# Optimization experiments

Hardware: AMD Instinct MI355X
Metric: run time of the kernel (lower is better)

Reference implementation:

```python
import math
import jax, jax.numpy as jnp
import numpy as np

L, B, N, D, H, DFF = 4, 64, 511, 256, 8, 512
S = N + 1          # +1 game token
HD = D // H
BW = 7             # BOARD_WIDTH (undefined global in source; board-game policy width)


def layer_norm(x, g, b):
    m = jnp.mean(x, axis=-1, keepdims=True)
    v = jnp.var(x, axis=-1, keepdims=True)
    return (x - m) / jnp.sqrt(v + 1e-5) * g + b


def setup_inputs() -> dict:
    key = jax.random.key(0)
    ks = jax.random.split(key, 24)

    def p(k, shape):
        return jax.random.normal(k, shape, jnp.float32) * 0.02

    return {
        "cell_states": jax.random.randint(ks[0], (B * N,), 0, 3, dtype=jnp.int32),
        "edge_type_matrix": jax.random.randint(ks[1], (B, N, N), 0, 3, dtype=jnp.int32),
        "patch_emb": p(ks[2], (3, D)),
        "game_token": p(ks[3], (1, 1, D)),
        "edge_emb": p(ks[4], (3, H)),   # zeros in source init; random here to exercise bias path
        "in_w": p(ks[5], (L, 3 * D, D)), "in_b": p(ks[6], (L, 3 * D)),
        "out_w": p(ks[7], (L, D, D)), "out_b": p(ks[8], (L, D)),
        "ff1_w": p(ks[9], (L, DFF, D)), "ff1_b": p(ks[10], (L, DFF)),
        "ff2_w": p(ks[11], (L, D, DFF)), "ff2_b": p(ks[12], (L, D)),
        "ln1_g": jnp.ones((L, D)), "ln1_b": jnp.zeros((L, D)),
        "ln2_g": jnp.ones((L, D)), "ln2_b": jnp.zeros((L, D)),
        "fc1_w": p(ks[13], (64, D)), "fc1_b": p(ks[14], (64,)),
        "pol_w": p(ks[15], (BW, 64)), "pol_b": p(ks[16], (BW,)),
        "val_w": p(ks[17], (1, 64)), "val_b": p(ks[18], (1,)),
    }


def reference(cell_states, edge_type_matrix, patch_emb, game_token, edge_emb,
              in_w, in_b, out_w, out_b, ff1_w, ff1_b, ff2_w, ff2_b,
              ln1_g, ln1_b, ln2_g, ln2_b, fc1_w, fc1_b, pol_w, pol_b, val_w, val_b):
    # embed cells and prepend game token -> [B, S, D]
    x = patch_emb[cell_states].reshape(B, N, D)
    x = jnp.concatenate([jnp.broadcast_to(game_token, (B, 1, D)), x], axis=1)

    # edge bias: [B,N,N,H] -> [B,H,N,N], pad token row/col with zeros -> [B,H,S,S]
    bias = jnp.transpose(edge_emb[edge_type_matrix], (0, 3, 1, 2))
    bias = jnp.pad(bias, ((0, 0), (0, 0), (1, 0), (1, 0)))

    scale = math.sqrt(HD)
    for i in range(L):
        h = layer_norm(x, ln1_g[i], ln1_b[i])
        qkv = h @ in_w[i].T + in_b[i]                       # [B,S,3D]
        q, k, v = jnp.split(qkv, 3, axis=-1)
        q = q.reshape(B, S, H, HD).transpose(0, 2, 1, 3)    # [B,H,S,HD]
        k = k.reshape(B, S, H, HD).transpose(0, 2, 1, 3)
        v = v.reshape(B, S, H, HD).transpose(0, 2, 1, 3)
        scores = jnp.einsum('bhqd,bhkd->bhqk', q, k) / scale + bias
        attn = jax.nn.softmax(scores, axis=-1)              # dropout = identity (eval)
        o = jnp.einsum('bhqk,bhkd->bhqd', attn, v)
        o = o.transpose(0, 2, 1, 3).reshape(B, S, D)
        x = x + (o @ out_w[i].T + out_b[i])
        h2 = layer_norm(x, ln2_g[i], ln2_b[i])
        x = x + (jax.nn.relu(h2 @ ff1_w[i].T + ff1_b[i]) @ ff2_w[i].T + ff2_b[i])

    g = x[:, 0, :]
    o = jax.nn.relu(g @ fc1_w.T + fc1_b)
    policy_logits = o @ pol_w.T + pol_b
    value = jnp.tanh(o @ val_w.T + val_b)
    return policy_logits, value
```

## Files before the change

### kernel.cpp

```cpp
#include <hip/hip_runtime.h>
#include <hip/hip_bf16.h>
#include <math.h>

#define L_ 4
#define B_ 64
#define N_ 511
#define D_ 256
#define H_ 8
#define DFF_ 512
#define S_ 512
#define HD_ 32
#define BW_ 7
#define BS_ (B_*S_)

typedef __attribute__((ext_vector_type(8))) short short8;
typedef __attribute__((ext_vector_type(4))) short short4v;
typedef __attribute__((ext_vector_type(4))) float f32x4;

#define L2E 1.44269504088896340f
#define QSCL (0.17677669529663687f * 1.44269504088896340f)

#if defined(__HIP_DEVICE_COMPILE__)
#if __has_builtin(__builtin_amdgcn_mfma_f32_16x16x16bf16_1k)
#define MFMA16(p, v, c) __builtin_amdgcn_mfma_f32_16x16x16bf16_1k(p, v, c, 0, 0, 0)
#elif __has_builtin(__builtin_amdgcn_mfma_f32_16x16x16_bf16)
#define MFMA16(p, v, c) __builtin_amdgcn_mfma_f32_16x16x16_bf16(p, v, c, 0, 0, 0)
#else
#define MFMA16(p, v, c) (c)
#endif
#else
#define MFMA16(p, v, c) (c)
#endif

#if defined(__HIP_DEVICE_COMPILE__) && __has_builtin(__builtin_amdgcn_exp2f)
#define EXP2(x) __builtin_amdgcn_exp2f(x)
#else
#define EXP2(x) exp2f(x)
#endif

__device__ inline ushort f2b(float f) {
    unsigned u = __float_as_uint(f);
    unsigned r = (u + 0x7fffu + ((u >> 16) & 1u)) >> 16;
    return (ushort)r;
}

#if defined(__HIP_DEVICE_COMPILE__) && __has_builtin(__builtin_amdgcn_cvt_pk_bf16_f32)
typedef __attribute__((ext_vector_type(2))) __bf16 bf16x2_t;
__device__ inline uint pk_bf16(float a, float b) {
    bf16x2_t r = __builtin_amdgcn_cvt_pk_bf16_f32(a, b);
    return *(uint*)&r;
}
#else
__device__ inline uint pk_bf16(float a, float b) {
    return (uint)f2b(a) | ((uint)f2b(b) << 16);
}
#endif

__device__ inline f32x4 bsel4v(uint E, uint tlo, uint thi) {
    f32x4 r;
#if defined(__HIP_DEVICE_COMPILE__) && __has_builtin(__builtin_amdgcn_perm)
    uint E2  = E + E;
    uint E2b = E2 | 0x01010101u;
    uint s01 = __builtin_amdgcn_perm(E2b, E2, 0x05010400u);
    uint s23 = __builtin_amdgcn_perm(E2b, E2, 0x07030602u);
    uint p01 = __builtin_amdgcn_perm(thi, tlo, s01);
    uint p23 = __builtin_amdgcn_perm(thi, tlo, s23);
    r[0] = __uint_as_float(p01 << 16);
    r[1] = __uint_as_float(p01 & 0xFFFF0000u);
    r[2] = __uint_as_float(p23 << 16);
    r[3] = __uint_as_float(p23 & 0xFFFF0000u);
#else
    #pragma unroll
    for (int i = 0; i < 4; i++) {
        unsigned char e = (unsigned char)((E >> (8 * i)) & 0xff);
        uint bb = e == 0 ? (tlo & 0xFFFFu) : (e == 1 ? (tlo >> 16) :
                  (e == 2 ? (thi & 0xFFFFu) : 0u));
        r[i] = __uint_as_float(bb << 16);
    }
#endif
    return r;
}

__device__ inline void gload16(const void* g, void* l) {
#if __has_builtin(__builtin_amdgcn_global_load_lds)
    __builtin_amdgcn_global_load_lds(
        (const __attribute__((address_space(1))) void*)g,
        (__attribute__((address_space(3))) void*)l, 16, 0, 0);
#else
    *(short8*)l = *(const short8*)g;
#endif
}

__global__ __launch_bounds__(256) void build_x(const int* __restrict__ cs,
                                               const float* __restrict__ patch,
                                               const float* __restrict__ game,
                                               float* __restrict__ x)
{
    int idx = blockIdx.x * 256 + threadIdx.x;
    int row = idx / (D_ / 4);
    int c4  = idx % (D_ / 4);
    int s = row & (S_ - 1);
    float4 v;
    if (s == 0) {
        v = ((const float4*)game)[c4];
    } else {
        int b = row / S_;
        int cell = cs[b * N_ + s - 1];
        v = ((const float4*)(patch + cell * D_))[c4];
    }
    ((float4*)x)[idx] = v;
}

__global__ __launch_bounds__(256) void build_et8(const int* __restrict__ et,
                                                 unsigned char* __restrict__ et8)
{
    long idx = (long)blockIdx.x * 256 + threadIdx.x;
    int k = (int)(idx & (S_ - 1));
    long rem = idx >> 9;
    int q = (int)(rem & (S_ - 1));
    int b = (int)(rem >> 9);
    unsigned char v = 3;
    if (q > 0 && k > 0) {
        v = (unsigned char)et[((long)b * N_ + (q - 1)) * N_ + (k - 1)];
    }
    et8[idx] = v;
}

__global__ __launch_bounds__(256) void convert_f2b(const float* __restrict__ in,
                                                   ushort* __restrict__ out, int n4)
{
    int i = blockIdx.x * 256 + threadIdx.x;
    if (i >= n4) return;
    float4 v = ((const float4*)in)[i];
    ushort4 o4;
    o4.x = f2b(v.x); o4.y = f2b(v.y); o4.z = f2b(v.z); o4.w = f2b(v.w);
    ((ushort4*)out)[i] = o4;
}

__global__ __launch_bounds__(256) void convert_inw(const float* __restrict__ in,
                                                   ushort* __restrict__ out)
{
    int i = blockIdx.x * 256 + threadIdx.x;
    if (i >= 196608) return;
    float4 v = ((const float4*)in)[i];
    int r = (i >> 6) % 768;
    float s = (r < 256) ? (float)QSCL : 1.f;
    ushort4 o4;
    o4.x = f2b(v.x * s); o4.y = f2b(v.y * s); o4.z = f2b(v.z * s); o4.w = f2b(v.w * s);
    ((ushort4*)out)[i] = o4;
}

__global__ __launch_bounds__(256) void ln_kernel(const float* __restrict__ in,
                                                 ushort* __restrict__ out,
                                                 const float* __restrict__ gw,
                                                 const float* __restrict__ bw)
{
    int t = threadIdx.x;
    int lane = t & 63;
    int r = t >> 6;
    size_t row = (size_t)blockIdx.x * 4 + r;
    float4 v = *(const float4*)(in + row * D_ + lane * 4);
    float s = v.x + v.y + v.z + v.w;
    #pragma unroll
    for (int o = 32; o >= 1; o >>= 1) s += __shfl_xor(s, o);
    float mean = s * (1.f / 256.f);
    float dx = v.x - mean, dy = v.y - mean, dz = v.z - mean, dw = v.w - mean;
    float s2 = dx * dx + dy * dy + dz * dz + dw * dw;
    #pragma unroll
    for (int o = 32; o >= 1; o >>= 1) s2 += __shfl_xor(s2, o);
    float rstd = rsqrtf(s2 * (1.f / 256.f) + 1e-5f);
    float4 g  = *(const float4*)(gw + lane * 4);
    float4 bb = *(const float4*)(bw + lane * 4);
    ushort4 o4;
    o4.x = f2b(dx * rstd * g.x + bb.x);
    o4.y = f2b(dy * rstd * g.y + bb.y);
    o4.z = f2b(dz * rstd * g.z + bb.z);
    o4.w = f2b(dw * rstd * g.w + bb.w);
    *(ushort4*)(out + row * D_ + lane * 4) = o4;
}

template<int K, int NT, bool RELU, bool QSC, bool QKV>
__global__ __launch_bounds__(256, 2) void gemm_lds(const ushort* __restrict__ A,
                                                   const ushort* __restrict__ W,
                                                   const float* __restrict__ bias,
                                                   ushort* __restrict__ Cout,
                                                   ushort* __restrict__ Kb,
                                                   ushort* __restrict__ Vt)
{
    __shared__ ushort As[4096];
    __shared__ ushort Ws[4096];
    const int N = NT * 128;
    int t = threadIdx.x;
    int wave = t >> 6, lane = t & 63;
    int lr = lane & 15, quad = lane >> 4;
    int lk = quad * 8;
    int blk = blockIdx.x;
    int xcd = blk & 7, idx = blk >> 3;
    int m0 = (xcd * 32 + (idx & 31)) * 128;
    int n0 = (idx >> 5) * 128;
    int mh = (wave >> 1) * 64, nh = (wave & 1) * 64;

    const ushort* ga0 = A + (size_t)(m0 + (t >> 2)) * K + (t & 3) * 8;
    const ushort* ga1 = ga0 + (size_t)64 * K;
    const ushort* gw0 = W + (size_t)(n0 + (t >> 2)) * K + (t & 3) * 8;
    const ushort* gw1 = gw0 + (size_t)64 * K;
    ushort* la0 = As + t * 8;
    ushort* la1 = As + t * 8 + 2048;
    ushort* lw0 = Ws + t * 8;
    ushort* lw1 = Ws + t * 8 + 2048;

    f32x4 acc[4][4];
    f32x4 zz = {0.f, 0.f, 0.f, 0.f};
    #pragma unroll
    for (int i = 0; i < 4; i++)
        #pragma unroll
        for (int j = 0; j < 4; j++) acc[i][j] = zz;

    for (int k0 = 0; k0 < K; k0 += 32) {
        gload16(ga0 + k0, la0);
        gload16(ga1 + k0, la1);
        gload16(gw0 + k0, lw0);
        gload16(gw1 + k0, lw1);
        __syncthreads();
        short8 af[4], wf[4];
        #pragma unroll
        for (int i = 0; i < 4; i++) af[i] = *(const short8*)&As[(mh + i * 16 + lr) * 32 + lk];
        #pragma unroll
        for (int j = 0; j < 4; j++) wf[j] = *(const short8*)&Ws[(nh + j * 16 + lr) * 32 + lk];
        #pragma unroll
        for (int i = 0; i < 4; i++)
            #pragma unroll
            for (int j = 0; j < 4; j++)
                acc[i][j] = __builtin_amdgcn_mfma_f32_16x16x32_bf16(af[i], wf[j], acc[i][j], 0, 0, 0);
        __syncthreads();
    }

    #pragma unroll
    for (int nt = 0; nt < 4; nt++) {
        int colbase = n0 + nh + nt * 16;
        int col = colbase + lr;
        float bv = bias[col];
        if (QSC && colbase < 256) bv *= (float)QSCL;
        int region = QKV ? (colbase >> 8) : 0;
        #pragma unroll
        for (int mt = 0; mt < 4; mt++) {
            int rowb = m0 + mh + mt * 16 + quad * 4;
            if (!QKV || region == 0) {
                #pragma unroll
                for (int r = 0; r < 4; r++) {
                    size_t cidx = (size_t)(rowb + r) * N + col;
                    float v = acc[mt][nt][r] + bv;
                    if (RELU) v = fmaxf(v, 0.f);
                    Cout[cidx] = f2b(v);
                }
            } else if (region == 1) {
                int hh = (col >> 5) & 7, d = col & 31;
                int bb = rowb >> 9, s = rowb & 511;
                size_t kbase = ((size_t)(bb * 8 + hh) * 512 + s) * 32 + d;
                #pragma unroll
                for (int r = 0; r < 4; r++)
                    Kb[kbase + (size_t)r * 32] = f2b(acc[mt][nt][r] + bv);
            } else {
                int hh = (col >> 5) & 7, d = col & 31;
                int bb = rowb >> 9, s = rowb & 511;
                ushort4 w;
                w.x = f2b(acc[mt][nt][0] + bv);
                w.y = f2b(acc[mt][nt][1] + bv);
                w.z = f2b(acc[mt][nt][2] + bv);
                w.w = f2b(acc[mt][nt][3] + bv);
                size_t vidx = (((size_t)(bb * 8 + hh) * 32 + (s >> 4)) * 32 + d) * 16 + (s & 15);
                *(ushort4*)&Vt[vidx] = w;
            }
        }
    }
}

template<int K>
__global__ __launch_bounds__(256, 2) void gemm_ln(const ushort* __restrict__ A,
                                                  const ushort* __restrict__ W,
                                                  const float* __restrict__ bias,
                                                  float* __restrict__ X,
                                                  const float* __restrict__ lng,
                                                  const float* __restrict__ lnb,
                                                  ushort* __restrict__ Hout)
{
    __shared__ ushort As[64 * 32];
    __shared__ ushort Ws[256 * 32];
    __shared__ float lds_s[64][4];
    __shared__ float lds_q[64][4];
    int t = threadIdx.x;
    int wave = t >> 6, lane = t & 63;
    int lr = lane & 15, quad = lane >> 4;
    int lk = quad * 8;
    int blk = blockIdx.x;
    int xcd = blk & 7;
    int m0 = (xcd * 64 + (blk >> 3)) * 64;
    int nh = wave * 64;

    const ushort* ga = A + (size_t)(m0 + (t >> 2)) * K + (t & 3) * 8;
    const ushort* gw = W + (size_t)(t >> 2) * K + (t & 3) * 8;
    ushort* la = As + t * 8;
    ushort* lw = Ws + t * 8;

    f32x4 acc[4][4];
    f32x4 zz = {0.f, 0.f, 0.f, 0.f};
    #pragma unroll
    for (int i = 0; i < 4; i++)
        #pragma unroll
        for (int j = 0; j < 4; j++) acc[i][j] = zz;

    for (int k0 = 0; k0 < K; k0 += 32) {
        gload16(ga + k0, la);
        #pragma unroll
        for (int j = 0; j < 4; j++)
            gload16(gw + (size_t)(j * 64) * K + k0, lw + j * 2048);
        __syncthreads();
        short8 af[4], wf[4];
        #pragma unroll
        for (int i = 0; i < 4; i++) af[i] = *(const short8*)&As[(i * 16 + lr) * 32 + lk];
        #pragma unroll
        for (int j = 0; j < 4; j++) wf[j] = *(const short8*)&Ws[(nh + j * 16 + lr) * 32 + lk];
        #pragma unroll
        for (int i = 0; i < 4; i++)
            #pragma unroll
            for (int j = 0; j < 4; j++)
                acc[i][j] = __builtin_amdgcn_mfma_f32_16x16x32_bf16(af[i], wf[j], acc[i][j], 0, 0, 0);
        __syncthreads();
    }

    float gc[4], bc[4], bi[4];
    #pragma unroll
    for (int nt = 0; nt < 4; nt++) {
        int col = nh + nt * 16 + lr;
        gc[nt] = lng[col]; bc[nt] = lnb[col]; bi[nt] = bias[col];
    }
    float psum[16], psq[16];
    #pragma unroll
    for (int e = 0; e < 16; e++) { psum[e] = 0.f; psq[e] = 0.f; }
    #pragma unroll
    for (int nt = 0; nt < 4; nt++) {
        #pragma unroll
        for (int mt = 0; mt < 4; mt++) {
            #pragma unroll
            for (int r = 0; r < 4; r++) {
                int row = m0 + mt * 16 + quad * 4 + r;
                size_t idx = (size_t)row * D_ + nh + nt * 16 + lr;
                float v = acc[mt][nt][r] + bi[nt] + X[idx];
                X[idx] = v;
                acc[mt][nt][r] = v;
                psum[mt * 4 + r] += v;
                psq[mt * 4 + r]  += v * v;
            }
        }
    }
    #pragma unroll
    for (int e = 0; e < 16; e++) {
        float s = psum[e], q = psq[e];
        s += __shfl_xor(s, 1); q += __shfl_xor(q, 1);
        s += __shfl_xor(s, 2); q += __shfl_xor(q, 2);
        s += __shfl_xor(s, 4); q += __shfl_xor(q, 4);
        s += __shfl_xor(s, 8); q += __shfl_xor(q, 8);
        psum[e] = s; psq[e] = q;
    }
    if (lr == 0) {
        #pragma unroll
        for (int mt = 0; mt < 4; mt++)
            #pragma unroll
            for (int r = 0; r < 4; r++) {
                int rl = mt * 16 + quad * 4 + r;
                lds_s[rl][wave] = psum[mt * 4 + r];
                lds_q[rl][wave] = psq[mt * 4 + r];
            }
    }
    __syncthreads();
    #pragma unroll
    for (int mt = 0; mt < 4; mt++) {
        #pragma unroll
        for (int r = 0; r < 4; r++) {
            int rl = mt * 16 + quad * 4 + r;
            f32x4 ss = *(const f32x4*)lds_s[rl];
            f32x4 qq = *(const f32x4*)lds_q[rl];
            float s = ss[0] + ss[1] + ss[2] + ss[3];
            float q = qq[0] + qq[1] + qq[2] + qq[3];
            float mean = s * (1.f / 256.f);
            float rstd = rsqrtf(q * (1.f / 256.f) - mean * mean + 1e-5f);
            int row = m0 + mt * 16 + quad * 4 + r;
            #pragma unroll
            for (int nt = 0; nt < 4; nt++) {
                size_t idx = (size_t)row * D_ + nh + nt * 16 + lr;
                float hv = (acc[mt][nt][r] - mean) * rstd * gc[nt] + bc[nt];
                Hout[idx] = f2b(hv);
            }
        }
    }
}

__global__ __launch_bounds__(256, 8) void attn_mfma(const ushort* __restrict__ qkv,
                                                    const ushort* __restrict__ Kb,
                                                    const ushort* __restrict__ Vt,
                                                    const unsigned char* __restrict__ et8,
                                                    const float* __restrict__ eemb,
                                                    ushort* __restrict__ o)
{
    __shared__ unsigned char Est[2][2][2048];
    int t = threadIdx.x;
    int wave = t >> 6, lane = t & 63;
    int lr = lane & 15, quad = lane >> 4;
    int lk = quad * 8;
    int blk = blockIdx.x;
    int b = ((blk >> 8) << 3) | (blk & 7);
    int h = (blk >> 3) & 7;
    int qq = (blk >> 6) & 3;
    int bh = b * 8 + h;
    int q0 = qq * 128 + wave * 32;
    float eb0 = eemb[h] * L2E, eb1 = eemb[8 + h] * L2E, eb2 = eemb[16 + h] * L2E;
    uint tlo = (uint)f2b(eb0) | ((uint)f2b(eb1) << 16);
    uint thi = (uint)f2b(eb2);

    short8 qf[2];
    #pragma unroll
    for (int X = 0; X < 2; X++)
        qf[X] = *(const short8*)(qkv + ((size_t)(b * S_ + q0 + X * 16 + lr)) * 768 + h * 32 + lk);
    const ushort* Kp = Kb + ((size_t)(bh * S_ + lr)) * 32 + lk;
    const ushort* Vp = Vt + (size_t)bh * 32 * 512 + lr * 16 + quad * 4;
    int ehalf = wave >> 1;
    int erow = ((wave & 1) << 6) | lane;
    const unsigned char* Ep = et8 + ((size_t)(b * S_ + qq * 128 + erow)) * S_ + ehalf * 16;
    unsigned char* ElD = &Est[0][ehalf][erow * 16];

    const short4v vones = { (short)0x3F80, (short)0x3F80, (short)0x3F80, (short)0x3F80 };

    f32x4 zz = {0.f, 0.f, 0.f, 0.f};
    f32x4 oacc[2][2], lacc[2];
    #pragma unroll
    for (int X = 0; X < 2; X++) { oacc[X][0] = zz; oacc[X][1] = zz; lacc[X] = zz; }

    gload16(Ep, ElD);
    short8 kf0 = *(const short8*)(Kp);
    short8 kf1 = *(const short8*)(Kp + 16 * 32);
    __syncthreads();

    for (int k0 = 0; k0 < S_; k0 += 32) {
        int cb = (k0 >> 5) & 1, nb = cb ^ 1;
        if (k0 < S_ - 32) {
            gload16(Ep + k0 + 32, ElD + (size_t)nb * 4096);
        }
        int kn = (k0 + 32) & (S_ - 1);
        short8 nk0 = *(const short8*)(Kp + (size_t)kn * 32);
        short8 nk1 = *(const short8*)(Kp + (size_t)(kn + 16) * 32);
        const ushort* vt0 = Vp + (size_t)(k0 >> 4) * 512;
        short4v vf00 = *(const short4v*)(vt0);
        short4v vf01 = *(const short4v*)(vt0 + 256);
        short4v vf10 = *(const short4v*)(vt0 + 512);
        short4v vf11 = *(const short4v*)(vt0 + 768);
        #pragma unroll
        for (int X = 0; X < 2; X++) {
            int qrow = wave * 32 + X * 16 + lr;
            uint E0 = *(const uint*)&Est[cb][0][qrow * 16 + quad * 4];
            uint E1 = *(const uint*)&Est[cb][1][qrow * 16 + quad * 4];
            f32x4 c0 = bsel4v(E0, tlo, thi);
            f32x4 c1 = bsel4v(E1, tlo, thi);
            f32x4 s0 = __builtin_amdgcn_mfma_f32_16x16x32_bf16(kf0, qf[X], c0, 0, 0, 0);
            f32x4 s1 = __builtin_amdgcn_mfma_f32_16x16x32_bf16(kf1, qf[X], c1, 0, 0, 0);
            float p0[4], p1[4];
            #pragma unroll
            for (int r = 0; r < 4; r++) {
                p0[r] = EXP2(s0[r]);
                p1[r] = EXP2(s1[r]);
            }
            union { short4v v; uint2 u; } P0, P1;
            P0.u.x = pk_bf16(p0[0], p0[1]); P0.u.y = pk_bf16(p0[2], p0[3]);
            P1.u.x = pk_bf16(p1[0], p1[1]); P1.u.y = pk_bf16(p1[2], p1[3]);
            oacc[X][0] = MFMA16(P0.v, vf00, oacc[X][0]);
            oacc[X][1] = MFMA16(P0.v, vf01, oacc[X][1]);
            lacc[X]    = MFMA16(P0.v, vones, lacc[X]);
            oacc[X][0] = MFMA16(P1.v, vf10, oacc[X][0]);
            oacc[X][1] = MFMA16(P1.v, vf11, oacc[X][1]);
            lacc[X]    = MFMA16(P1.v, vones, lacc[X]);
        }
        kf0 = nk0; kf1 = nk1;
        __syncthreads();
    }

    #pragma unroll
    for (int X = 0; X < 2; X++) {
        #pragma unroll
        for (int r = 0; r < 4; r++) {
            int q = quad * 4 + r;
            float inv = 1.f / lacc[X][r];
            size_t base = (size_t)(b * S_ + q0 + X * 16 + q) * D_ + h * 32;
            o[base + lr]      = f2b(oacc[X][0][r] * inv);
            o[base + 16 + lr] = f2b(oacc[X][1][r] * inv);
        }
    }
}

__global__ __launch_bounds__(64) void head_kernel(const float* __restrict__ x,
                                                  const float* __restrict__ fc1w,
                                                  const float* __restrict__ fc1b,
                                                  const float* __restrict__ polw,
                                                  const float* __restrict__ polb,
                                                  const float* __restrict__ valw,
                                                  const float* __restrict__ valb,
                                                  float* __restrict__ out)
{
    __shared__ float o1[64];
    int b = blockIdx.x;
    int t = threadIdx.x;
    const float* g = x + (size_t)b * S_ * D_;
    float acc = fc1b[t];
    for (int k = 0; k < D_; k++) acc += g[k] * fc1w[t * D_ + k];
    o1[t] = fmaxf(acc, 0.f);
    __syncthreads();
    if (t < BW_) {
        float a = polb[t];
        for (int k = 0; k < 64; k++) a += o1[k] * polw[t * 64 + k];
        out[b * BW_ + t] = a;
    } else if (t == BW_) {
        float a = valb[0];
        for (int k = 0; k < 64; k++) a += o1[k] * valw[k];
        out[B_ * BW_ + b] = tanhf(a);
    }
}

extern "C" void kernel_launch(void* const* d_in, const int* in_sizes, int n_in,
                              void* d_out, int out_size, void* d_ws, size_t ws_size,
                              hipStream_t stream)
{
    const int*   cs    = (const int*)d_in[0];
    const int*   etm   = (const int*)d_in[1];
    const float* patch = (const float*)d_in[2];
    const float* game  = (const float*)d_in[3];
    const float* eemb  = (const float*)d_in[4];
    const float* in_w  = (const float*)d_in[5];
    const float* in_b  = (const float*)d_in[6];
    const float* out_w = (const float*)d_in[7];
    const float* out_b = (const float*)d_in[8];
    const float* ff1_w = (const float*)d_in[9];
    const float* ff1_b = (const float*)d_in[10];
    const float* ff2_w = (const float*)d_in[11];
    const float* ff2_b = (const float*)d_in[12];
    const float* ln1_g = (const float*)d_in[13];
    const float* ln1_b = (const float*)d_in[14];
    const float* ln2_g = (const float*)d_in[15];
    const float* ln2_b = (const float*)d_in[16];
    const float* fc1_w = (const float*)d_in[17];
    const float* fc1_b = (const float*)d_in[18];
    const float* pol_w = (const float*)d_in[19];
    const float* pol_b = (const float*)d_in[20];
    const float* val_w = (const float*)d_in[21];
    const float* val_b = (const float*)d_in[22];
    float* out = (float*)d_out;

    char* base = (char*)d_ws;
    float*  x     = (float*)(base + 0);
    ushort* h     = (ushort*)(base + 33554432);
    ushort* qkvb  = (ushort*)(base + 50331648);
    ushort* Kb    = (ushort*)(base + 100663296);
    ushort* Vt    = (ushort*)(base + 117440512);
    ushort* ob    = (ushort*)(base + 134217728);
    unsigned char* et8 = (unsigned char*)(base + 150994944);
    ushort* inwb  = (ushort*)(base + 167772160);
    ushort* outwb = (ushort*)(base + 169345024);
    ushort* ff1wb = (ushort*)(base + 169869312);
    ushort* ff2wb = (ushort*)(base + 170917888);

    build_x<<<8192, 256, 0, stream>>>(cs, patch, game, x);
    build_et8<<<65536, 256, 0, stream>>>(etm, et8);
    convert_inw<<<768, 256, 0, stream>>>(in_w, inwb);
    convert_f2b<<<256, 256, 0, stream>>>(out_w, outwb, 65536);
    convert_f2b<<<512, 256, 0, stream>>>(ff1_w, ff1wb, 131072);
    convert_f2b<<<512, 256, 0, stream>>>(ff2_w, ff2wb, 131072);

    ln_kernel<<<8192, 256, 0, stream>>>(x, h, ln1_g, ln1_b);

    for (int i = 0; i < L_; i++) {
        gemm_lds<256, 6, false, true, true><<<1536, 256, 0, stream>>>(
            h, inwb + (size_t)i * 196608, in_b + i * 768, qkvb, Kb, Vt);
        attn_mfma<<<2048, 256, 0, stream>>>(qkvb, Kb, Vt, et8, eemb, ob);
        gemm_ln<256><<<512, 256, 0, stream>>>(
            ob, outwb + (size_t)i * 65536, out_b + i * 256, x,
            ln2_g + i * D_, ln2_b + i * D_, h);
        gemm_lds<256, 4, true, false, false><<<1024, 256, 0, stream>>>(
            h, ff1wb + (size_t)i * 131072, ff1_b + i * 512, qkvb, nullptr, nullptr);
        int nx = (i + 1 < L_) ? (i + 1) : i;
        gemm_ln<512><<<512, 256, 0, stream>>>(
            qkvb, ff2wb + (size_t)i * 131072, ff2_b + i * 256, x,
            ln1_g + nx * D_, ln1_b + nx * D_, h);
    }
    head_kernel<<<B_, 64, 0, stream>>>(x, fc1_w, fc1_b, pol_w, pol_b, val_w, val_b, out);
}
```

Baseline: 801.7 us.

## Use 16x16x32 MFMA for PV with permuted K rows and direct edge loads

Result: slower. 1.993 ms (+148.6%).

```diff
diff --git a/kernel.cpp b/kernel.cpp
--- a/kernel.cpp
+++ b/kernel.cpp
@@ -19,18 +19,6 @@
 
 #define L2E 1.44269504088896340f
 #define QSCL (0.17677669529663687f * 1.44269504088896340f)
-
-#if defined(__HIP_DEVICE_COMPILE__)
-#if __has_builtin(__builtin_amdgcn_mfma_f32_16x16x16bf16_1k)
-#define MFMA16(p, v, c) __builtin_amdgcn_mfma_f32_16x16x16bf16_1k(p, v, c, 0, 0, 0)
-#elif __has_builtin(__builtin_amdgcn_mfma_f32_16x16x16_bf16)
-#define MFMA16(p, v, c) __builtin_amdgcn_mfma_f32_16x16x16_bf16(p, v, c, 0, 0, 0)
-#else
-#define MFMA16(p, v, c) (c)
-#endif
-#else
-#define MFMA16(p, v, c) (c)
-#endif
 
 #if defined(__HIP_DEVICE_COMPILE__) && __has_builtin(__builtin_amdgcn_exp2f)
 #define EXP2(x) __builtin_amdgcn_exp2f(x)
@@ -402,7 +390,6 @@
                                                     const float* __restrict__ eemb,
                                                     ushort* __restrict__ o)
 {
-    __shared__ unsigned char Est[2][2][2048];
     int t = threadIdx.x;
     int wave = t >> 6, lane = t & 63;
     int lr = lane & 15, quad = lane >> 4;
@@ -421,45 +408,40 @@
     #pragma unroll
     for (int X = 0; X < 2; X++)
         qf[X] = *(const short8*)(qkv + ((size_t)(b * S_ + q0 + X * 16 + lr)) * 768 + h * 32 + lk);
-    const ushort* Kp = Kb + ((size_t)(bh * S_ + lr)) * 32 + lk;
-    const ushort* Vp = Vt + (size_t)bh * 32 * 512 + lr * 16 + quad * 4;
-    int ehalf = wave >> 1;
-    int erow = ((wave & 1) << 6) | lane;
-    const unsigned char* Ep = et8 + ((size_t)(b * S_ + qq * 128 + erow)) * S_ + ehalf * 16;
-    unsigned char* ElD = &Est[0][ehalf][erow * 16];
-
-    const short4v vones = { (short)0x3F80, (short)0x3F80, (short)0x3F80, (short)0x3F80 };
+    int gl = ((lr >> 2) << 3) | (lr & 3);
+    const ushort* Kp = Kb + ((size_t)(bh * S_) + gl) * 32 + lk;
+    const ushort* Vp = Vt + (size_t)bh * 16384 + (quad >> 1) * 512 + lr * 16 + (quad & 1) * 8;
+    const unsigned char* Ep0 = et8 + ((size_t)(b * S_ + q0 + lr)) * 512 + quad * 8;
+    const unsigned char* Ep1 = Ep0 + (size_t)16 * 512;
+
+    const short8 vones8 = { (short)0x3F80, (short)0x3F80, (short)0x3F80, (short)0x3F80,
+                            (short)0x3F80, (short)0x3F80, (short)0x3F80, (short)0x3F80 };
 
     f32x4 zz = {0.f, 0.f, 0.f, 0.f};
     f32x4 oacc[2][2], lacc[2];
     #pragma unroll
     for (int X = 0; X < 2; X++) { oacc[X][0] = zz; oacc[X][1] = zz; lacc[X] = zz; }
 
-    gload16(Ep, ElD);
     short8 kf0 = *(const short8*)(Kp);
-    short8 kf1 = *(const short8*)(Kp + 16 * 32);
-    __syncthreads();
+    short8 kf1 = *(const short8*)(Kp + 128);
+    uint2 e0 = *(const uint2*)(Ep0);
+    uint2 e1 = *(const uint2*)(Ep1);
 
     for (int k0 = 0; k0 < S_; k0 += 32) {
-        int cb = (k0 >> 5) & 1, nb = cb ^ 1;
-        if (k0 < S_ - 32) {
-            gload16(Ep + k0 + 32, ElD + (size_t)nb * 4096);
-        }
         int kn = (k0 + 32) & (S_ - 1);
         short8 nk0 = *(const short8*)(Kp + (size_t)kn * 32);
-        short8 nk1 = *(const short8*)(Kp + (size_t)(kn + 16) * 32);
+        short8 nk1 = *(const short8*)(Kp + (size_t)kn * 32 + 128);
+        uint2 ne0 = *(const uint2*)(Ep0 + kn);
+        uint2 ne1 = *(const uint2*)(Ep1 + kn);
         const ushort* vt0 = Vp + (size_t)(k0 >> 4) * 512;
-        short4v vf00 = *(const short4v*)(vt0);
-        short4v vf01 = *(const short4v*)(vt0 + 256);
-        short4v vf10 = *(const short4v*)(vt0 + 512);
-        short4v vf11 = *(const short4v*)(vt0 + 768);
+        short8 vb0 = *(const short8*)(vt0);
+        short8 vb1 = *(const short8*)(vt0 + 256);
         #pragma unroll
         for (int X = 0; X < 2; X++) {
-            int qrow = wave * 32 + X * 16 + lr;
-            uint E0 = *(const uint*)&Est[cb][0][qrow * 16 + quad * 4];
-            uint E1 = *(const uint*)&Est[cb][1][qrow * 16 + quad * 4];
-            f32x4 c0 = bsel4v(E0, tlo, thi);
-            f32x4 c1 = bsel4v(E1, tlo, thi);
+            uint Ea = X ? e1.x : e0.x;
+            uint Eb = X ? e1.y : e0.y;
+            f32x4 c0 = bsel4v(Ea, tlo, thi);
+            f32x4 c1 = bsel4v(Eb, tlo, thi);
             f32x4 s0 = __builtin_amdgcn_mfma_f32_16x16x32_bf16(kf0, qf[X], c0, 0, 0, 0);
             f32x4 s1 = __builtin_amdgcn_mfma_f32_16x16x32_bf16(kf1, qf[X], c1, 0, 0, 0);
             float p0[4], p1[4];
@@ -468,18 +450,14 @@
                 p0[r] = EXP2(s0[r]);
                 p1[r] = EXP2(s1[r]);
             }
-            union { short4v v; uint2 u; } P0, P1;
-            P0.u.x = pk_bf16(p0[0], p0[1]); P0.u.y = pk_bf16(p0[2], p0[3]);
-            P1.u.x = pk_bf16(p1[0], p1[1]); P1.u.y = pk_bf16(p1[2], p1[3]);
-            oacc[X][0] = MFMA16(P0.v, vf00, oacc[X][0]);
-            oacc[X][1] = MFMA16(P0.v, vf01, oacc[X][1]);
-            lacc[X]    = MFMA16(P0.v, vones, lacc[X]);
-            oacc[X][0] = MFMA16(P1.v, vf10, oacc[X][0]);
-            oacc[X][1] = MFMA16(P1.v, vf11, oacc[X][1]);
-            lacc[X]    = MFMA16(P1.v, vones, lacc[X]);
+            union { short8 v; uint u[4]; } PA;
+            PA.u[0] = pk_bf16(p0[0], p0[1]); PA.u[1] = pk_bf16(p0[2], p0[3]);
+            PA.u[2] = pk_bf16(p1[0], p1[1]); PA.u[3] = pk_bf16(p1[2], p1[3]);
+            oacc[X][0] = __builtin_amdgcn_mfma_f32_16x16x32_bf16(PA.v, vb0, oacc[X][0], 0, 0, 0);
+            oacc[X][1] = __builtin_amdgcn_mfma_f32_16x16x32_bf16(PA.v, vb1, oacc[X][1], 0, 0, 0);
+            lacc[X]    = __builtin_amdgcn_mfma_f32_16x16x32_bf16(PA.v, vones8, lacc[X], 0, 0, 0);
         }
-        kf0 = nk0; kf1 = nk1;
-        __syncthreads();
+        kf0 = nk0; kf1 = nk1; e0 = ne0; e1 = ne1;
     }
 
     #pragma unroll
```
